# Kernel optimization log

Measured on AMD Instinct MI355X. Metric: run time of the kernel, lower is better.

The kernel has to match this reference:

```python
import jax, jax.numpy as jnp
import numpy as np

DIM = 1024
NUM_HEADS = 16
HEAD_DIM = DIM // NUM_HEADS
SCALE = HEAD_DIM ** -0.5
B, LQ, LK = 2, 2048, 2048


def setup_inputs() -> dict:
    key = jax.random.key(0)
    ks = jax.random.split(key, 12)
    init = 1.0 / np.sqrt(DIM)  # ~ torch Linear default scale
    inp = {
        "q": jax.random.normal(ks[0], (B, LQ, DIM), jnp.float32),
        "k": jax.random.normal(ks[1], (B, LK, DIM), jnp.float32),
        "v": jax.random.normal(ks[2], (B, LK, DIM), jnp.float32),
        "kv_mask": jnp.ones((B, LK), jnp.int32),
        "Wq": jax.random.uniform(ks[3], (DIM, DIM), jnp.float32, -init, init),
        "bq": jax.random.uniform(ks[4], (DIM,), jnp.float32, -init, init),
        "Wk": jax.random.uniform(ks[5], (DIM, DIM), jnp.float32, -init, init),
        "bk": jax.random.uniform(ks[6], (DIM,), jnp.float32, -init, init),
        "Wv": jax.random.uniform(ks[7], (DIM, DIM), jnp.float32, -init, init),
        "bv": jax.random.uniform(ks[8], (DIM,), jnp.float32, -init, init),
        "Wo": jax.random.uniform(ks[9], (DIM, DIM), jnp.float32, -init, init),
        "bo": jax.random.uniform(ks[10], (DIM,), jnp.float32, -init, init),
    }
    return inp


def reference(q, k, v, kv_mask, Wq, bq, Wk, bk, Wv, bv, Wo, bo):
    Bq, Lq, D = q.shape
    Lk = k.shape[1]
    H, Hd = NUM_HEADS, HEAD_DIM
    # projections (torch Linear: x @ W.T + b); split heads -> [B, H, L, Hd]
    qh = (q @ Wq.T + bq).reshape(Bq, Lq, H, Hd).transpose(0, 2, 1, 3)
    kh = (k @ Wk.T + bk).reshape(Bq, Lk, H, Hd).transpose(0, 2, 1, 3)
    vh = (v @ Wv.T + bv).reshape(Bq, Lk, H, Hd).transpose(0, 2, 1, 3)
    # scores [B, H, Lq, Lk]
    attn = jnp.einsum("bhqd,bhkd->bhqk", qh, kh) * SCALE
    mask = (kv_mask != 0)[:, None, None, :]
    attn = jnp.where(mask, attn, -jnp.inf)
    attn = jax.nn.softmax(attn, axis=-1)
    # dropout is identity at inference (p applied only in train mode)
    out = jnp.einsum("bhqk,bhkd->bhqd", attn, vh)
    out = out.transpose(0, 2, 1, 3).reshape(Bq, Lq, D)
    return out @ Wo.T + bo
```

## Files before the change

kernel.cpp:

```cpp
#include <hip/hip_runtime.h>
#include <stdint.h>

typedef unsigned short u16;
typedef __attribute__((ext_vector_type(8))) __bf16 bf16x8;
typedef __attribute__((ext_vector_type(4))) float f32x4;

#define DIM 1024
#define NH 16
#define HD 64
#define BSZ 2
#define LQ 2048
#define LK 2048
#define SCALE_LOG2E 0.18033688011112043f
#define FLAG_THRESH 8192
#define MNEG -3.0e38f

static __device__ __forceinline__ float b2f(u16 u) {
  union { uint32_t i; float f; } v; v.i = ((uint32_t)u) << 16; return v.f;
}
static __device__ __forceinline__ u16 f2b(float f) {
  uint32_t x = __float_as_uint(f);
  return (u16)((x + 0x7fffu + ((x >> 16) & 1u)) >> 16);
}
static __device__ __forceinline__ uint32_t pk2(float lo, float hi) {
  return (uint32_t)f2b(lo) | ((uint32_t)f2b(hi) << 16);
}
static __device__ __forceinline__ f32x4 zero4() {
  f32x4 z; z[0] = 0.f; z[1] = 0.f; z[2] = 0.f; z[3] = 0.f; return z;
}
static __device__ __forceinline__ void gload_lds16(const u16* g, u16* l) {
  __builtin_amdgcn_global_load_lds(
      (const __attribute__((address_space(1))) void*)g,
      (__attribute__((address_space(3))) void*)l, 16, 0, 0);
}

__global__ void detect_dtype(const u16* q, int* cnt) {
  int i = blockIdx.x * blockDim.x + threadIdx.x;
  u16 u = q[2 * i];
  int e = (u >> 7) & 0xFF;
  unsigned long long m = __ballot(e >= 0x90);
  if ((threadIdx.x & 63) == 0) atomicAdd(cnt, (int)__popcll(m));
}

struct ConvArgs {
  const void* src[11];
  long long cum[12];
  const int* flag;
  u16* dst;
};

__global__ void convert_inputs(ConvArgs ca) {
  const bool f32 = (*ca.flag) > FLAG_THRESH;
  long long c = (long long)blockIdx.x * blockDim.x + threadIdx.x;
  long long e0 = c * 8;
  if (e0 >= ca.cum[11]) return;
  int s = 0;
  while (e0 >= ca.cum[s + 1]) ++s;
  long long local = e0 - ca.cum[s];
  union { uint4 v; u16 h[8]; } t;
  if (f32) {
    const float* sp = (const float*)ca.src[s] + local;
#pragma unroll
    for (int j = 0; j < 8; ++j) t.h[j] = f2b(sp[j]);
  } else {
    t.v = *(const uint4*)((const u16*)ca.src[s] + local);
  }
  *(uint4*)(ca.dst + e0) = t.v;
}

struct GemmArgs {
  const u16* X[3];
  const u16* W[3];
  const u16* Bias[3];
  void* Y[3];
  const int* flag;
  int vtz;
};

__global__ __launch_bounds__(256, 2) void gemm_bt_bias(GemmArgs ga) {
  const int K = DIM, N = DIM;
  __shared__ u16 Al[128 * 64];
  __shared__ u16 Bl[128 * 64];
  const int tid = threadIdx.x;
  const int wave = tid >> 6, lane = tid & 63;
  const int wm = wave >> 1, wn = wave & 1;
  const int lrow = lane & 15, quad = lane >> 4;
  const int z = blockIdx.z;
  const u16* X = ga.X[z];
  const u16* W = ga.W[z];
  const u16* Bias = ga.Bias[z];
  const int m0 = blockIdx.x * 128;
  const int n0 = blockIdx.y * 128;

  f32x4 acc[4][4];
#pragma unroll
  for (int i = 0; i < 4; ++i)
#pragma unroll
    for (int j = 0; j < 4; ++j) acc[i][j] = zero4();

  const int cbase = wave * 256;
  for (int k0 = 0; k0 < K; k0 += 64) {
    __syncthreads();
#pragma unroll
    for (int i = 0; i < 4; ++i) {
      int c = cbase + i * 64 + lane;
      int row = c >> 3, colb = c & 7;
      gload_lds16(X + (size_t)(m0 + row) * K + k0 + colb * 8,
                  &Al[(cbase + i * 64) * 8]);
      gload_lds16(W + (size_t)(n0 + row) * K + k0 + colb * 8,
                  &Bl[(cbase + i * 64) * 8]);
    }
    __syncthreads();
#pragma unroll
    for (int ks = 0; ks < 2; ++ks) {
      bf16x8 af[4], bfr[4];
#pragma unroll
      for (int t = 0; t < 4; ++t)
        af[t] = *(const bf16x8*)&Al[(wm * 64 + t * 16 + lrow) * 64 + ks * 32 + quad * 8];
#pragma unroll
      for (int t = 0; t < 4; ++t)
        bfr[t] = *(const bf16x8*)&Bl[(wn * 64 + t * 16 + lrow) * 64 + ks * 32 + quad * 8];
#pragma unroll
      for (int mt = 0; mt < 4; ++mt)
#pragma unroll
        for (int nt = 0; nt < 4; ++nt)
          acc[mt][nt] = __builtin_amdgcn_mfma_f32_16x16x32_bf16(af[mt], bfr[nt], acc[mt][nt], 0, 0, 0);
    }
  }

  const bool f32out = (ga.flag != nullptr) && (*ga.flag > FLAG_THRESH);
  void* Yv = ga.Y[z];
  if (z == ga.vtz) {
#pragma unroll
    for (int nt = 0; nt < 4; ++nt) {
      int col = n0 + wn * 64 + nt * 16 + lrow;
      float bv = b2f(Bias[col]);
      int hh = col >> 6, dd = col & 63;
#pragma unroll
      for (int mt = 0; mt < 4; ++mt) {
        int rowb = m0 + wm * 64 + mt * 16 + quad * 4;
        int bb = rowb >> 11, key = rowb & 2047;
        uint2 w;
        w.x = pk2(acc[mt][nt][0] + bv, acc[mt][nt][1] + bv);
        w.y = pk2(acc[mt][nt][2] + bv, acc[mt][nt][3] + bv);
        *(uint2*)((u16*)Yv + ((size_t)(bb * NH + hh) * HD + dd) * LK + key) = w;
      }
    }
  } else {
#pragma unroll
    for (int nt = 0; nt < 4; ++nt) {
      int col = n0 + wn * 64 + nt * 16 + lrow;
      float bv = b2f(Bias[col]);
#pragma unroll
      for (int mt = 0; mt < 4; ++mt) {
        int rowb = m0 + wm * 64 + mt * 16 + quad * 4;
#pragma unroll
        for (int r = 0; r < 4; ++r) {
          float val = acc[mt][nt][r] + bv;
          size_t idx = (size_t)(rowb + r) * N + col;
          if (f32out) ((float*)Yv)[idx] = val;
          else        ((u16*)Yv)[idx] = f2b(val);
        }
      }
    }
  }
}

__global__ __launch_bounds__(256, 2) void attn_fused(
    const u16* __restrict__ qp, const u16* __restrict__ kp,
    const u16* __restrict__ vpt, const int* __restrict__ kvmask,
    u16* __restrict__ op) {
  __shared__ u16 Kl[128 * 72];
  __shared__ u16 Vt[64 * 136];
  __shared__ u16 Pq[4][32 * 136];
  __shared__ float Ml[128];
  const int tid = threadIdx.x;
  const int wave = tid >> 6, lane = tid & 63;
  const int lrow = lane & 15, quad = lane >> 4;
  const int bh = blockIdx.y;
  const int b = bh >> 4, h = bh & 15;
  const int q0 = blockIdx.x * 128;

  const u16* qbase = qp + (size_t)b * LQ * DIM + h * HD;
  const u16* kbase = kp + (size_t)b * LK * DIM + h * HD;
  const u16* vtb = vpt + (size_t)(b * NH + h) * HD * LK;
  const int* mbase = kvmask + b * LK;
  const int wq0 = q0 + wave * 32;

  bf16x8 qf[2][2];
#pragma unroll
  for (int mt = 0; mt < 2; ++mt)
#pragma unroll
    for (int ks = 0; ks < 2; ++ks)
      qf[mt][ks] = *(const bf16x8*)(qbase + (size_t)(wq0 + mt * 16 + lrow) * DIM + ks * 32 + quad * 8);

  f32x4 acco[2][4];
  float mrow[2], lsum[2];
#pragma unroll
  for (int mt = 0; mt < 2; ++mt) {
#pragma unroll
    for (int dt = 0; dt < 4; ++dt) acco[mt][dt] = zero4();
    mrow[mt] = MNEG; lsum[mt] = 0.0f;
  }

  for (int kc = 0; kc < LK; kc += 128) {
    __syncthreads();
#pragma unroll
    for (int i = 0; i < 4; ++i) {
      int c = i * 256 + tid;
      int row = c >> 3, colb = c & 7;
      *(uint4*)&Kl[row * 72 + colb * 8] =
          *(const uint4*)(kbase + (size_t)(kc + row) * DIM + colb * 8);
      int d = c >> 4, k8 = c & 15;
      *(uint4*)&Vt[d * 136 + k8 * 8] =
          *(const uint4*)(vtb + (size_t)d * LK + kc + k8 * 8);
    }
    if (tid < 128) Ml[tid] = mbase[kc + tid] ? 0.0f : MNEG;
    __syncthreads();

    f32x4 sacc[2][8];
#pragma unroll
    for (int mt = 0; mt < 2; ++mt)
#pragma unroll
      for (int nt = 0; nt < 8; ++nt) sacc[mt][nt] = zero4();
#pragma unroll
    for (int ks = 0; ks < 2; ++ks) {
#pragma unroll
      for (int nt = 0; nt < 8; ++nt) {
        bf16x8 kf = *(const bf16x8*)&Kl[(nt * 16 + lrow) * 72 + ks * 32 + quad * 8];
        sacc[0][nt] = __builtin_amdgcn_mfma_f32_16x16x32_bf16(kf, qf[0][ks], sacc[0][nt], 0, 0, 0);
        sacc[1][nt] = __builtin_amdgcn_mfma_f32_16x16x32_bf16(kf, qf[1][ks], sacc[1][nt], 0, 0, 0);
      }
    }

    u16* pqw = &Pq[wave][0];
#pragma unroll
    for (int mt = 0; mt < 2; ++mt) {
      float mx = MNEG;
#pragma unroll
      for (int nt = 0; nt < 8; ++nt) {
        f32x4 mq = *(const f32x4*)&Ml[nt * 16 + quad * 4];
#pragma unroll
        for (int r = 0; r < 4; ++r) {
          float s = fmaf(sacc[mt][nt][r], SCALE_LOG2E, mq[r]);
          sacc[mt][nt][r] = s;
          mx = fmaxf(mx, s);
        }
      }
      mx = fmaxf(mx, __shfl_xor(mx, 16));
      mx = fmaxf(mx, __shfl_xor(mx, 32));
      float mnew = fmaxf(mrow[mt], mx);
      float alpha = exp2f(mrow[mt] - mnew);
      mrow[mt] = mnew;
      float rsum = 0.0f;
      u16* prow = &pqw[(mt * 16 + lrow) * 136];
#pragma unroll
      for (int nt = 0; nt < 8; ++nt) {
        float p0 = exp2f(sacc[mt][nt][0] - mnew);
        float p1 = exp2f(sacc[mt][nt][1] - mnew);
        float p2 = exp2f(sacc[mt][nt][2] - mnew);
        float p3 = exp2f(sacc[mt][nt][3] - mnew);
        rsum += (p0 + p1) + (p2 + p3);
        uint2 w; w.x = pk2(p0, p1); w.y = pk2(p2, p3);
        *(uint2*)&prow[nt * 16 + quad * 4] = w;
      }
      rsum += __shfl_xor(rsum, 16);
      rsum += __shfl_xor(rsum, 32);
      lsum[mt] = lsum[mt] * alpha + rsum;
#pragma unroll
      for (int dt = 0; dt < 4; ++dt) {
        acco[mt][dt][0] *= alpha; acco[mt][dt][1] *= alpha;
        acco[mt][dt][2] *= alpha; acco[mt][dt][3] *= alpha;
      }
    }

#pragma unroll
    for (int kb = 0; kb < 4; ++kb) {
      bf16x8 pf0 = *(const bf16x8*)&pqw[(0 * 16 + lrow) * 136 + kb * 32 + quad * 8];
      bf16x8 pf1 = *(const bf16x8*)&pqw[(1 * 16 + lrow) * 136 + kb * 32 + quad * 8];
#pragma unroll
      for (int dt = 0; dt < 4; ++dt) {
        bf16x8 vf = *(const bf16x8*)&Vt[(dt * 16 + lrow) * 136 + kb * 32 + quad * 8];
        acco[0][dt] = __builtin_amdgcn_mfma_f32_16x16x32_bf16(vf, pf0, acco[0][dt], 0, 0, 0);
        acco[1][dt] = __builtin_amdgcn_mfma_f32_16x16x32_bf16(vf, pf1, acco[1][dt], 0, 0, 0);
      }
    }
  }

  u16* ob = op + (size_t)b * LQ * DIM + h * HD;
#pragma unroll
  for (int mt = 0; mt < 2; ++mt) {
    float inv = lsum[mt] > 0.0f ? 1.0f / lsum[mt] : 0.0f;
    int q = wq0 + mt * 16 + lrow;
#pragma unroll
    for (int dt = 0; dt < 4; ++dt) {
      uint2 w;
      w.x = pk2(acco[mt][dt][0] * inv, acco[mt][dt][1] * inv);
      w.y = pk2(acco[mt][dt][2] * inv, acco[mt][dt][3] * inv);
      *(uint2*)&ob[(size_t)q * DIM + dt * 16 + quad * 4] = w;
    }
  }
}

extern "C" void kernel_launch(void* const* d_in, const int* in_sizes, int n_in,
                              void* d_out, int out_size, void* d_ws, size_t ws_size,
                              hipStream_t stream) {
  (void)in_sizes; (void)n_in; (void)out_size; (void)ws_size;
  const int* kvmask = (const int*)d_in[3];

  u16* ws = (u16*)d_ws;
  const long long SQ = (long long)BSZ * LQ * DIM;
  const long long SW = (long long)DIM * DIM;
  const long long SB = DIM;
  long long cum[12];
  cum[0] = 0;
  cum[1] = cum[0] + SQ;
  cum[2] = cum[1] + SQ;
  cum[3] = cum[2] + SQ;
  cum[4] = cum[3] + SW;
  cum[5] = cum[4] + SW;
  cum[6] = cum[5] + SW;
  cum[7] = cum[6] + SW;
  cum[8] = cum[7] + SB;
  cum[9] = cum[8] + SB;
  cum[10] = cum[9] + SB;
  cum[11] = cum[10] + SB;
  const long long canon_end = cum[11];
  u16* cq  = ws + cum[0];
  u16* ck  = ws + cum[1];
  u16* cv  = ws + cum[2];
  u16* cWq = ws + cum[3];
  u16* cWk = ws + cum[4];
  u16* cWv = ws + cum[5];
  u16* cWo = ws + cum[6];
  u16* cbq = ws + cum[7];
  u16* cbk = ws + cum[8];
  u16* cbv = ws + cum[9];
  u16* cbo = ws + cum[10];
  u16* qp  = ws + canon_end;
  u16* kp  = qp + SQ;
  u16* vpt = kp + SQ;
  u16* ao  = vpt + SQ;
  int* flag = (int*)(ao + SQ);

  hipMemsetAsync(flag, 0, sizeof(int), stream);
  detect_dtype<<<256, 256, 0, stream>>>((const u16*)d_in[0], flag);

  ConvArgs ca;
  ca.src[0] = d_in[0];  ca.src[1] = d_in[1];  ca.src[2] = d_in[2];
  ca.src[3] = d_in[4];  ca.src[4] = d_in[6];  ca.src[5] = d_in[8];
  ca.src[6] = d_in[10]; ca.src[7] = d_in[5];  ca.src[8] = d_in[7];
  ca.src[9] = d_in[9];  ca.src[10] = d_in[11];
  for (int i = 0; i < 12; ++i) ca.cum[i] = cum[i];
  ca.flag = flag;
  ca.dst = ws;
  int conv_blocks = (int)((canon_end / 8 + 255) / 256);
  convert_inputs<<<conv_blocks, 256, 0, stream>>>(ca);

  const int M = BSZ * LQ;

  GemmArgs g1;
  g1.X[0] = cq; g1.W[0] = cWq; g1.Bias[0] = cbq; g1.Y[0] = qp;
  g1.X[1] = ck; g1.W[1] = cWk; g1.Bias[1] = cbk; g1.Y[1] = kp;
  g1.X[2] = cv; g1.W[2] = cWv; g1.Bias[2] = cbv; g1.Y[2] = vpt;
  g1.flag = nullptr;
  g1.vtz = 2;
  gemm_bt_bias<<<dim3(M / 128, DIM / 128, 3), dim3(256), 0, stream>>>(g1);

  attn_fused<<<dim3(LQ / 128, BSZ * NH), dim3(256), 0, stream>>>(qp, kp, vpt, kvmask, ao);

  GemmArgs g2;
  g2.X[0] = ao; g2.W[0] = cWo; g2.Bias[0] = cbo; g2.Y[0] = d_out;
  g2.X[1] = ao; g2.W[1] = cWo; g2.Bias[1] = cbo; g2.Y[1] = d_out;
  g2.X[2] = ao; g2.W[2] = cWo; g2.Bias[2] = cbo; g2.Y[2] = d_out;
  g2.flag = flag;
  g2.vtz = -1;
  gemm_bt_bias<<<dim3(M / 128, DIM / 128, 1), dim3(256), 0, stream>>>(g2);
}
```

Measured before the change: 282.2 us.

## Fold softmax scale into Q projection, skip mask when all valid, stage V transpose via LDS

The 1/sqrt(d) scale is folded into the Q projection epilogue, and the attention kernel now uses natural-log scores with an FMA into exp2. A small pre-pass checks whether every key-value mask entry is valid; when it is, the attention kernel skips loading and adding the mask. The V-projection epilogue now stages its transposed tile in shared memory so the global stores are coalesced 16-byte writes instead of scattered 8-byte ones. BF16 packing switches to a cheaper round-half-up form using a byte permute, which changes rounding slightly compared with round-to-nearest-even.

```diff
diff --git a/kernel.cpp b/kernel.cpp
--- a/kernel.cpp
+++ b/kernel.cpp
@@ -11,7 +11,7 @@
 #define BSZ 2
 #define LQ 2048
 #define LK 2048
-#define SCALE_LOG2E 0.18033688011112043f
+#define LOG2E 1.4426950408889634f
 #define FLAG_THRESH 8192
 #define MNEG -3.0e38f
 
@@ -22,8 +22,10 @@
   uint32_t x = __float_as_uint(f);
   return (u16)((x + 0x7fffu + ((x >> 16) & 1u)) >> 16);
 }
-static __device__ __forceinline__ uint32_t pk2(float lo, float hi) {
-  return (uint32_t)f2b(lo) | ((uint32_t)f2b(hi) << 16);
+static __device__ __forceinline__ uint32_t pk2r(float lo, float hi) {
+  uint32_t a = __float_as_uint(lo) + 0x8000u;
+  uint32_t b = __float_as_uint(hi) + 0x8000u;
+  return __builtin_amdgcn_perm(b, a, 0x07060302u);
 }
 static __device__ __forceinline__ f32x4 zero4() {
   f32x4 z; z[0] = 0.f; z[1] = 0.f; z[2] = 0.f; z[3] = 0.f; return z;
@@ -40,6 +42,16 @@
   int e = (u >> 7) & 0xFF;
   unsigned long long m = __ballot(e >= 0x90);
   if ((threadIdx.x & 63) == 0) atomicAdd(cnt, (int)__popcll(m));
+}
+
+__global__ void mask_allvalid(const int* __restrict__ kvmask, int* allv) {
+  int b = blockIdx.x;
+  int base = b * LK + threadIdx.x * 8;
+  int ok = 1;
+#pragma unroll
+  for (int j = 0; j < 8; ++j) ok &= (kvmask[base + j] != 0);
+  unsigned long long m = __ballot(ok != 0);
+  if ((threadIdx.x & 63) == 0 && m != ~0ULL) atomicAnd(&allv[b], 0);
 }
 
 struct ConvArgs {
@@ -73,14 +85,16 @@
   const u16* W[3];
   const u16* Bias[3];
   void* Y[3];
+  float osc[3];
   const int* flag;
   int vtz;
 };
 
 __global__ __launch_bounds__(256, 2) void gemm_bt_bias(GemmArgs ga) {
   const int K = DIM, N = DIM;
-  __shared__ u16 Al[128 * 64];
-  __shared__ u16 Bl[128 * 64];
+  __shared__ u16 smem[17408];
+  u16* const Al = smem;
+  u16* const Bl = smem + 8192;
   const int tid = threadIdx.x;
   const int wave = tid >> 6, lane = tid & 63;
   const int wm = wave >> 1, wn = wave & 1;
@@ -89,6 +103,7 @@
   const u16* X = ga.X[z];
   const u16* W = ga.W[z];
   const u16* Bias = ga.Bias[z];
+  const float osc = ga.osc[z];
   const int m0 = blockIdx.x * 128;
   const int n0 = blockIdx.y * 128;
 
@@ -128,35 +143,45 @@
     }
   }
 
-  const bool f32out = (ga.flag != nullptr) && (*ga.flag > FLAG_THRESH);
   void* Yv = ga.Y[z];
   if (z == ga.vtz) {
+    u16* const VT = smem;
+    __syncthreads();
+#pragma unroll
+    for (int nt = 0; nt < 4; ++nt) {
+      int colL = wn * 64 + nt * 16 + lrow;
+      float bv = b2f(Bias[n0 + colL]);
+#pragma unroll
+      for (int mt = 0; mt < 4; ++mt) {
+        int keyL = wm * 64 + mt * 16 + quad * 4;
+        uint2 w;
+        w.x = pk2r((acc[mt][nt][0] + bv) * osc, (acc[mt][nt][1] + bv) * osc);
+        w.y = pk2r((acc[mt][nt][2] + bv) * osc, (acc[mt][nt][3] + bv) * osc);
+        *(uint2*)&VT[colL * 136 + keyL] = w;
+      }
+    }
+    __syncthreads();
+    const int bb = m0 >> 11, key0 = m0 & 2047;
+#pragma unroll
+    for (int i = 0; i < 8; ++i) {
+      int c = i * 256 + tid;
+      int colL = c >> 4, k8 = c & 15;
+      int hh = (n0 + colL) >> 6, dd = (n0 + colL) & 63;
+      *(uint4*)((u16*)Yv + ((size_t)(bb * NH + hh) * HD + dd) * LK + key0 + k8 * 8) =
+          *(const uint4*)&VT[colL * 136 + k8 * 8];
+    }
+  } else {
+    const bool f32out = (ga.flag != nullptr) && (*ga.flag > FLAG_THRESH);
 #pragma unroll
     for (int nt = 0; nt < 4; ++nt) {
       int col = n0 + wn * 64 + nt * 16 + lrow;
       float bv = b2f(Bias[col]);
-      int hh = col >> 6, dd = col & 63;
 #pragma unroll
       for (int mt = 0; mt < 4; ++mt) {
         int rowb = m0 + wm * 64 + mt * 16 + quad * 4;
-        int bb = rowb >> 11, key = rowb & 2047;
-        uint2 w;
-        w.x = pk2(acc[mt][nt][0] + bv, acc[mt][nt][1] + bv);
-        w.y = pk2(acc[mt][nt][2] + bv, acc[mt][nt][3] + bv);
-        *(uint2*)((u16*)Yv + ((size_t)(bb * NH + hh) * HD + dd) * LK + key) = w;
-      }
-    }
-  } else {
-#pragma unroll
-    for (int nt = 0; nt < 4; ++nt) {
-      int col = n0 + wn * 64 + nt * 16 + lrow;
-      float bv = b2f(Bias[col]);
-#pragma unroll
-      for (int mt = 0; mt < 4; ++mt) {
-        int rowb = m0 + wm * 64 + mt * 16 + quad * 4;
 #pragma unroll
         for (int r = 0; r < 4; ++r) {
-          float val = acc[mt][nt][r] + bv;
+          float val = (acc[mt][nt][r] + bv) * osc;
           size_t idx = (size_t)(rowb + r) * N + col;
           if (f32out) ((float*)Yv)[idx] = val;
           else        ((u16*)Yv)[idx] = f2b(val);
@@ -169,7 +194,7 @@
 __global__ __launch_bounds__(256, 2) void attn_fused(
     const u16* __restrict__ qp, const u16* __restrict__ kp,
     const u16* __restrict__ vpt, const int* __restrict__ kvmask,
-    u16* __restrict__ op) {
+    const int* __restrict__ allv, u16* __restrict__ op) {
   __shared__ u16 Kl[128 * 72];
   __shared__ u16 Vt[64 * 136];
   __shared__ u16 Pq[4][32 * 136];
@@ -180,6 +205,7 @@
   const int bh = blockIdx.y;
   const int b = bh >> 4, h = bh & 15;
   const int q0 = blockIdx.x * 128;
+  const bool av = (allv[b] != 0);
 
   const u16* qbase = qp + (size_t)b * LQ * DIM + h * HD;
   const u16* kbase = kp + (size_t)b * LK * DIM + h * HD;
@@ -215,7 +241,7 @@
       *(uint4*)&Vt[d * 136 + k8 * 8] =
           *(const uint4*)(vtb + (size_t)d * LK + kc + k8 * 8);
     }
-    if (tid < 128) Ml[tid] = mbase[kc + tid] ? 0.0f : MNEG;
+    if (!av && tid < 128) Ml[tid] = mbase[kc + tid] ? 0.0f : MNEG;
     __syncthreads();
 
     f32x4 sacc[2][8];
@@ -237,31 +263,40 @@
 #pragma unroll
     for (int mt = 0; mt < 2; ++mt) {
       float mx = MNEG;
-#pragma unroll
-      for (int nt = 0; nt < 8; ++nt) {
-        f32x4 mq = *(const f32x4*)&Ml[nt * 16 + quad * 4];
-#pragma unroll
-        for (int r = 0; r < 4; ++r) {
-          float s = fmaf(sacc[mt][nt][r], SCALE_LOG2E, mq[r]);
-          sacc[mt][nt][r] = s;
-          mx = fmaxf(mx, s);
+      if (av) {
+#pragma unroll
+        for (int nt = 0; nt < 8; ++nt) {
+#pragma unroll
+          for (int r = 0; r < 4; ++r) mx = fmaxf(mx, sacc[mt][nt][r]);
+        }
+      } else {
+#pragma unroll
+        for (int nt = 0; nt < 8; ++nt) {
+          f32x4 mq = *(const f32x4*)&Ml[nt * 16 + quad * 4];
+#pragma unroll
+          for (int r = 0; r < 4; ++r) {
+            float s = sacc[mt][nt][r] + mq[r];
+            sacc[mt][nt][r] = s;
+            mx = fmaxf(mx, s);
+          }
         }
       }
       mx = fmaxf(mx, __shfl_xor(mx, 16));
       mx = fmaxf(mx, __shfl_xor(mx, 32));
       float mnew = fmaxf(mrow[mt], mx);
-      float alpha = exp2f(mrow[mt] - mnew);
+      float alpha = exp2f((mrow[mt] - mnew) * LOG2E);
       mrow[mt] = mnew;
+      float cc = -fmaxf(mnew, -1e30f) * LOG2E;
       float rsum = 0.0f;
       u16* prow = &pqw[(mt * 16 + lrow) * 136];
 #pragma unroll
       for (int nt = 0; nt < 8; ++nt) {
-        float p0 = exp2f(sacc[mt][nt][0] - mnew);
-        float p1 = exp2f(sacc[mt][nt][1] - mnew);
-        float p2 = exp2f(sacc[mt][nt][2] - mnew);
-        float p3 = exp2f(sacc[mt][nt][3] - mnew);
+        float p0 = exp2f(fmaf(sacc[mt][nt][0], LOG2E, cc));
+        float p1 = exp2f(fmaf(sacc[mt][nt][1], LOG2E, cc));
+        float p2 = exp2f(fmaf(sacc[mt][nt][2], LOG2E, cc));
+        float p3 = exp2f(fmaf(sacc[mt][nt][3], LOG2E, cc));
         rsum += (p0 + p1) + (p2 + p3);
-        uint2 w; w.x = pk2(p0, p1); w.y = pk2(p2, p3);
+        uint2 w; w.x = pk2r(p0, p1); w.y = pk2r(p2, p3);
         *(uint2*)&prow[nt * 16 + quad * 4] = w;
       }
       rsum += __shfl_xor(rsum, 16);
@@ -295,8 +330,8 @@
 #pragma unroll
     for (int dt = 0; dt < 4; ++dt) {
       uint2 w;
-      w.x = pk2(acco[mt][dt][0] * inv, acco[mt][dt][1] * inv);
-      w.y = pk2(acco[mt][dt][2] * inv, acco[mt][dt][3] * inv);
+      w.x = pk2r(acco[mt][dt][0] * inv, acco[mt][dt][1] * inv);
+      w.y = pk2r(acco[mt][dt][2] * inv, acco[mt][dt][3] * inv);
       *(uint2*)&ob[(size_t)q * DIM + dt * 16 + quad * 4] = w;
     }
   }
@@ -342,9 +377,12 @@
   u16* vpt = kp + SQ;
   u16* ao  = vpt + SQ;
   int* flag = (int*)(ao + SQ);
+  int* allv = flag + 2;
 
   hipMemsetAsync(flag, 0, sizeof(int), stream);
+  hipMemsetAsync(allv, 0xFF, 2 * sizeof(int), stream);
   detect_dtype<<<256, 256, 0, stream>>>((const u16*)d_in[0], flag);
+  mask_allvalid<<<BSZ, 256, 0, stream>>>(kvmask, allv);
 
   ConvArgs ca;
   ca.src[0] = d_in[0];  ca.src[1] = d_in[1];  ca.src[2] = d_in[2];
@@ -363,16 +401,20 @@
   g1.X[0] = cq; g1.W[0] = cWq; g1.Bias[0] = cbq; g1.Y[0] = qp;
   g1.X[1] = ck; g1.W[1] = cWk; g1.Bias[1] = cbk; g1.Y[1] = kp;
   g1.X[2] = cv; g1.W[2] = cWv; g1.Bias[2] = cbv; g1.Y[2] = vpt;
+  g1.osc[0] = 0.125f;
+  g1.osc[1] = 1.0f;
+  g1.osc[2] = 1.0f;
   g1.flag = nullptr;
   g1.vtz = 2;
   gemm_bt_bias<<<dim3(M / 128, DIM / 128, 3), dim3(256), 0, stream>>>(g1);
 
-  attn_fused<<<dim3(LQ / 128, BSZ * NH), dim3(256), 0, stream>>>(qp, kp, vpt, kvmask, ao);
+  attn_fused<<<dim3(LQ / 128, BSZ * NH), dim3(256), 0, stream>>>(qp, kp, vpt, kvmask, allv, ao);
 
   GemmArgs g2;
   g2.X[0] = ao; g2.W[0] = cWo; g2.Bias[0] = cbo; g2.Y[0] = d_out;
   g2.X[1] = ao; g2.W[1] = cWo; g2.Bias[1] = cbo; g2.Y[1] = d_out;
   g2.X[2] = ao; g2.W[2] = cWo; g2.Bias[2] = cbo; g2.Y[2] = d_out;
+  g2.osc[0] = 1.0f; g2.osc[1] = 1.0f; g2.osc[2] = 1.0f;
   g2.flag = flag;
   g2.vtz = -1;
   gemm_bt_bias<<<dim3(M / 128, DIM / 128, 1), dim3(256), 0, stream>>>(g2);
```

Result: faster. 271.2 us (-3.9%).
